# Kernel optimization log

Hardware: AMD Instinct MI355X
Metric: run time of the kernel (lower is better)

Reference implementation:

```python
import jax, jax.numpy as jnp
import numpy as np

N = 50000   # nodes
E = 400000  # edges
H = 4       # heads
C = 64      # hidden per head
IN = 8
G = 64      # graphs in batch
NEG_SLOPE = 0.2


def setup_inputs() -> dict:
    key = jax.random.key(0)
    ks = jax.random.split(key, 32)
    def w(k, shape, fan_in):
        return jax.random.normal(k, shape, jnp.float32) * (1.0 / np.sqrt(fan_in))
    inp = {}
    inp['x'] = jax.random.normal(ks[0], (N, IN), jnp.float32)
    inp['edge_index'] = jax.random.randint(ks[1], (2, E), 0, N, jnp.int32)
    inp['edge_attr'] = jax.random.normal(ks[2], (E, 1), jnp.float32)
    inp['batch'] = jnp.sort(jax.random.randint(ks[3], (N,), 0, G, jnp.int32))
    # encoder
    inp['enc_w'] = w(ks[4], (IN, H * 16), IN)[:, :64]  # [8,64]
    inp['enc_b'] = jnp.zeros((64,), jnp.float32)
    # gat1: in 64 -> H*C = 256
    inp['g1_wl'] = w(ks[5], (64, H * C), 64)
    inp['g1_bl'] = jnp.zeros((H * C,), jnp.float32)
    inp['g1_wr'] = w(ks[6], (64, H * C), 64)
    inp['g1_we'] = w(ks[7], (1, H * C), 1)
    inp['g1_att'] = w(ks[8], (H, C), C)
    inp['g1_b'] = jnp.zeros((H * C,), jnp.float32)
    # gat2: in 256 -> H*C = 256
    inp['g2_wl'] = w(ks[9], (H * C, H * C), H * C)
    inp['g2_bl'] = jnp.zeros((H * C,), jnp.float32)
    inp['g2_wr'] = w(ks[10], (H * C, H * C), H * C)
    inp['g2_we'] = w(ks[11], (1, H * C), 1)
    inp['g2_att'] = w(ks[12], (H, C), C)
    inp['g2_b'] = jnp.zeros((H * C,), jnp.float32)
    # post MLP: 256 -> 128 -> LN -> ReLU -> 128 -> 64 -> ReLU
    inp['p1_w'] = w(ks[13], (H * C, 128), H * C)
    inp['p1_b'] = jnp.zeros((128,), jnp.float32)
    inp['ln_g'] = jnp.ones((128,), jnp.float32)
    inp['ln_b'] = jnp.zeros((128,), jnp.float32)
    inp['p2_w'] = w(ks[14], (128, 64), 128)
    inp['p2_b'] = jnp.zeros((64,), jnp.float32)
    inp['head_w'] = w(ks[15], (64, 1), 64)
    inp['head_b'] = jnp.zeros((1,), jnp.float32)
    return inp


def gatv2_conv(h, src, dst, ea, wl, bl, wr, we, att, b):
    # PyG GATv2Conv (concat=True): message from src j aggregated at dst i
    xl = (h @ wl + bl).reshape(N, H, C)   # lin_l(x_j), carries source messages
    xr = (h @ wr).reshape(N, H, C)        # lin_r(x_i)
    e = (ea @ we).reshape(E, H, C)        # lin_edge(edge_attr)
    s = jax.nn.leaky_relu(xl[src] + xr[dst] + e, NEG_SLOPE)  # [E,H,C]
    logits = jnp.einsum('ehc,hc->eh', s, att)                # [E,H]
    # softmax over incoming edges of each dst node
    mx = jax.ops.segment_max(logits, dst, num_segments=N)
    ex = jnp.exp(logits - mx[dst])
    denom = jax.ops.segment_sum(ex, dst, num_segments=N)
    alpha = ex / (denom[dst] + 1e-16)                        # [E,H]
    out = jax.ops.segment_sum(alpha[:, :, None] * xl[src], dst, num_segments=N)
    return out.reshape(N, H * C) + b


def reference(x, edge_index, edge_attr, batch, enc_w, enc_b,
              g1_wl, g1_bl, g1_wr, g1_we, g1_att, g1_b,
              g2_wl, g2_bl, g2_wr, g2_we, g2_att, g2_b,
              p1_w, p1_b, ln_g, ln_b, p2_w, p2_b, head_w, head_b):
    src, dst = edge_index[0], edge_index[1]
    h = jax.nn.relu(x @ enc_w + enc_b)
    h = jax.nn.relu(gatv2_conv(h, src, dst, edge_attr, g1_wl, g1_bl, g1_wr, g1_we, g1_att, g1_b))
    h = jax.nn.relu(gatv2_conv(h, src, dst, edge_attr, g2_wl, g2_bl, g2_wr, g2_we, g2_att, g2_b))
    # global mean pool per graph
    s = jax.ops.segment_sum(h, batch, num_segments=G)
    cnt = jax.ops.segment_sum(jnp.ones((N,), h.dtype), batch, num_segments=G)
    g = s / jnp.maximum(cnt, 1.0)[:, None]                   # [G, H*C]
    # post MLP (dropout is identity in eval)
    z = g @ p1_w + p1_b
    mu = jnp.mean(z, axis=-1, keepdims=True)
    var = jnp.mean((z - mu) ** 2, axis=-1, keepdims=True)
    z = (z - mu) * jax.lax.rsqrt(var + 1e-5) * ln_g + ln_b
    z = jax.nn.relu(z)
    z = jax.nn.relu(z @ p2_w + p2_b)
    return (z @ head_w + head_b).squeeze(-1)                 # [G]
```

## Files before the change

kernel.cpp:

```cpp
#include <hip/hip_runtime.h>
#include <hip/hip_bf16.h>
#include <math.h>

#define NN 50000
#define NE 400000
#define HH 4
#define CC 64
#define HC 256
#define GG 64
#define NB 196
#define ENCB 12500
#define WCB 640

typedef short v8s __attribute__((ext_vector_type(8)));
typedef float f32x4 __attribute__((ext_vector_type(4)));

static __device__ inline unsigned short f2bf(float v) {
  __hip_bfloat16 b = __float2bfloat16(v);
  return *reinterpret_cast<unsigned short*>(&b);
}
static __device__ inline float bflo(unsigned u) { return __uint_as_float(u << 16); }
static __device__ inline float bfhi(unsigned u) { return __uint_as_float(u & 0xffff0000u); }

__global__ __launch_bounds__(256) void head_kernel(
    const float* __restrict__ x, const float* __restrict__ enc_w,
    const float* __restrict__ enc_b, unsigned short* __restrict__ h0,
    const float* __restrict__ g1_wl, const float* __restrict__ g1_wr,
    const float* __restrict__ g2_wl, const float* __restrict__ g2_wr,
    unsigned short* __restrict__ wt1, unsigned short* __restrict__ wt2,
    const int* __restrict__ batch, int* __restrict__ deg,
    float* __restrict__ pool, int* __restrict__ bounds) {
  int bid = blockIdx.x, tid = threadIdx.x;
  if (bid < ENCB) {
    int idx = bid * 256 + tid;
    int node = idx >> 6, col = idx & 63;
    const float* xr = x + node * 8;
    float acc = enc_b[col];
#pragma unroll
    for (int k = 0; k < 8; ++k) acc += xr[k] * enc_w[k * 64 + col];
    h0[idx] = f2bf(fmaxf(acc, 0.f));
  } else if (bid < ENCB + WCB) {
    int idx = (bid - ENCB) * 256 + tid;
    const float* W; unsigned short* Wt; int K; int base;
    if (idx < 16384)        { W = g1_wl; Wt = wt1;                     K = 64;  base = idx; }
    else if (idx < 32768)   { W = g1_wr; Wt = wt1 + (size_t)256 * 64;  K = 64;  base = idx - 16384; }
    else if (idx < 98304)   { W = g2_wl; Wt = wt2;                     K = 256; base = idx - 32768; }
    else if (idx < 163840)  { W = g2_wr; Wt = wt2 + (size_t)256 * 256; K = 256; base = idx - 98304; }
    else return;
    int k = base >> 8, n = base & 255;
    Wt[n * K + k] = f2bf(W[base]);
  } else {
    int sb = bid - ENCB - WCB;
    int i = sb * 256 + tid;
    if (i < NN) deg[i] = 0;
    if (sb < GG) pool[sb * 256 + tid] = 0.f;
    if (sb == NB - 1 && tid <= GG) {
      int g = tid, lo = 0, hi = NN;
      while (lo < hi) {
        int mid = (lo + hi) >> 1;
        if (batch[mid] < g) lo = mid + 1; else hi = mid;
      }
      bounds[g] = lo;
    }
  }
}

template <int K>
__global__ __launch_bounds__(256) void matmul_mfma_kernel(
    const unsigned short* __restrict__ A, const unsigned short* __restrict__ Wt,
    const float* __restrict__ bias,
    unsigned short* __restrict__ outL, unsigned short* __restrict__ outR, int M) {
  constexpr int AP = 40;
  __shared__ unsigned short a_lds[128 * AP];
  __shared__ unsigned short b_lds[128 * AP];
  const int tid = threadIdx.x;
  const int wave = tid >> 6;
  const int lane = tid & 63;
  const int quad = lane >> 4;
  const int lrow = lane & 15;
  const int wr = (wave & 1) * 64;
  const int wc = (wave >> 1) * 64;
  const int r0 = blockIdx.x * 128;
  const int n0 = blockIdx.y * 128;

  f32x4 acc[4][4];
#pragma unroll
  for (int i = 0; i < 4; ++i)
#pragma unroll
    for (int j = 0; j < 4; ++j) acc[i][j] = (f32x4){0.f, 0.f, 0.f, 0.f};

  const int srow = tid >> 1;
  const int shalf = tid & 1;
  int agrow = r0 + srow; if (agrow >= M) agrow = M - 1;
  const int bgrow = n0 + srow;

  for (int k0 = 0; k0 < K; k0 += 32) {
    {
      const float4* sa = (const float4*)&A[(size_t)agrow * K + k0 + shalf * 16];
      const float4* sb = (const float4*)&Wt[(size_t)bgrow * K + k0 + shalf * 16];
      float4 va0 = sa[0], va1 = sa[1];
      float4 vb0 = sb[0], vb1 = sb[1];
      *(float4*)&a_lds[srow * AP + shalf * 16]     = va0;
      *(float4*)&a_lds[srow * AP + shalf * 16 + 8] = va1;
      *(float4*)&b_lds[srow * AP + shalf * 16]     = vb0;
      *(float4*)&b_lds[srow * AP + shalf * 16 + 8] = vb1;
    }
    __syncthreads();

    v8s af[4], bf[4];
#pragma unroll
    for (int rt = 0; rt < 4; ++rt)
      af[rt] = *(const v8s*)&a_lds[(wr + rt * 16 + lrow) * AP + quad * 8];
#pragma unroll
    for (int ct = 0; ct < 4; ++ct)
      bf[ct] = *(const v8s*)&b_lds[(wc + ct * 16 + lrow) * AP + quad * 8];
#pragma unroll
    for (int rt = 0; rt < 4; ++rt)
#pragma unroll
      for (int ct = 0; ct < 4; ++ct)
        acc[rt][ct] = __builtin_amdgcn_mfma_f32_16x16x32_bf16(af[rt], bf[ct], acc[rt][ct], 0, 0, 0);
    __syncthreads();
  }

  const bool isL = (n0 < 256);
  unsigned short* outp = isL ? outL : outR;
  const int cbase = isL ? n0 : (n0 - 256);
  constexpr int SP = 136;
  unsigned short* stage = a_lds;

#pragma unroll
  for (int rt = 0; rt < 4; ++rt) {
    __syncthreads();
#pragma unroll
    for (int ct = 0; ct < 4; ++ct) {
      int col = wc + ct * 16 + lrow;
      float b = isL ? bias[cbase + col] : 0.f;
#pragma unroll
      for (int r = 0; r < 4; ++r) {
        int sr = (wave & 1) * 16 + quad * 4 + r;
        stage[sr * SP + col] = f2bf(acc[rt][ct][r] + b);
      }
    }
    __syncthreads();
    int sr = tid >> 3;
    int c0 = (tid & 7) * 16;
    int grow = r0 + (sr >> 4) * 64 + rt * 16 + (sr & 15);
    if (grow < M) {
      uint4 v0 = *(const uint4*)&stage[sr * SP + c0];
      uint4 v1 = *(const uint4*)&stage[sr * SP + c0 + 8];
      *(uint4*)&outp[(size_t)grow * 256 + cbase + c0] = v0;
      *(uint4*)&outp[(size_t)grow * 256 + cbase + c0 + 8] = v1;
    }
  }
}

__global__ void degree_kernel(const int* __restrict__ ei, int* __restrict__ deg) {
  int e = blockIdx.x * 256 + threadIdx.x;
  if (e < NE) atomicAdd(&deg[ei[NE + e]], 1);
}

__global__ __launch_bounds__(256) void blocksum_kernel(
    const int* __restrict__ deg, int* __restrict__ bsum) {
  int t = threadIdx.x;
  int i = blockIdx.x * 256 + t;
  int v = (i < NN) ? deg[i] : 0;
#pragma unroll
  for (int off = 32; off; off >>= 1) v += __shfl_down(v, off, 64);
  __shared__ int ws[4];
  if ((t & 63) == 0) ws[t >> 6] = v;
  __syncthreads();
  if (t == 0) bsum[blockIdx.x] = ws[0] + ws[1] + ws[2] + ws[3];
}

__global__ __launch_bounds__(256) void blockscan_kernel(
    const int* __restrict__ bsum, int* __restrict__ bpre, int* __restrict__ rowstart) {
  __shared__ int s[256];
  int t = threadIdx.x;
  int v = (t < NB) ? bsum[t] : 0;
  s[t] = v;
  __syncthreads();
  for (int off = 1; off < 256; off <<= 1) {
    int x = s[t];
    int y = (t >= off) ? s[t - off] : 0;
    __syncthreads();
    s[t] = x + y;
    __syncthreads();
  }
  if (t < NB) bpre[t] = s[t] - v;
  if (t == 255) rowstart[NN] = s[255];
}

__global__ __launch_bounds__(256) void rowstart_kernel(
    const int* __restrict__ deg, const int* __restrict__ bpre,
    int* __restrict__ rowstart, int* __restrict__ cursor) {
  __shared__ int s[256];
  int t = threadIdx.x;
  int i = blockIdx.x * 256 + t;
  int v = (i < NN) ? deg[i] : 0;
  s[t] = v;
  __syncthreads();
  for (int off = 1; off < 256; off <<= 1) {
    int x = s[t];
    int y = (t >= off) ? s[t - off] : 0;
    __syncthreads();
    s[t] = x + y;
    __syncthreads();
  }
  if (i < NN) {
    int rs = bpre[blockIdx.x] + s[t] - v;
    rowstart[i] = rs;
    cursor[i] = rs;
  }
}

__global__ void fill_kernel(const int* __restrict__ ei, const float* __restrict__ ea,
                            int* __restrict__ cursor, int2* __restrict__ edges) {
  int e = blockIdx.x * 256 + threadIdx.x;
  if (e < NE) {
    int d = ei[NE + e];
    int pos = atomicAdd(&cursor[d], 1);
    edges[pos] = make_int2(ei[e] << 9, __float_as_int(ea[e]));
  }
}

__global__ __launch_bounds__(256) void gat_fused_kernel(
    const int* __restrict__ rowstart, const int2* __restrict__ edges,
    const unsigned short* __restrict__ xl, const unsigned short* __restrict__ xr,
    const float* __restrict__ we, const float* __restrict__ att,
    const float* __restrict__ bias, unsigned short* __restrict__ outb) {
  int node = (blockIdx.x * 256 + threadIdx.x) >> 6;
  int lane = threadIdx.x & 63;
  int r0 = __builtin_amdgcn_readfirstlane(rowstart[node]);
  int r1 = __builtin_amdgcn_readfirstlane(rowstart[node + 1]);
  const char* xlp = (const char*)xl + lane * 8;
  uint2 rp = ((const uint2*)xr)[(size_t)node * 64 + lane];
  float4 r = make_float4(bflo(rp.x), bfhi(rp.x), bflo(rp.y), bfhi(rp.y));
  float4 wv = ((const float4*)we)[lane];
  float4 at = ((const float4*)att)[lane];
  const float LOG2E = 1.442695040888963f;
  at.x *= LOG2E; at.y *= LOG2E; at.z *= LOG2E; at.w *= LOG2E;
  float4 acc = make_float4(0.f, 0.f, 0.f, 0.f);
  float denom = 0.f;

  auto edge_step = [&](float eav, uint2 p) {
    float4 a = make_float4(bflo(p.x), bfhi(p.x), bflo(p.y), bfhi(p.y));
    float s0 = a.x + (r.x + eav * wv.x);
    float s1 = a.y + (r.y + eav * wv.y);
    float s2 = a.z + (r.z + eav * wv.z);
    float s3 = a.w + (r.w + eav * wv.w);
    s0 = fmaxf(s0, 0.2f * s0);
    s1 = fmaxf(s1, 0.2f * s1);
    s2 = fmaxf(s2, 0.2f * s2);
    s3 = fmaxf(s3, 0.2f * s3);
    float p4 = (s0 * at.x + s1 * at.y) + (s2 * at.z + s3 * at.w);
#pragma unroll
    for (int off = 8; off; off >>= 1) p4 += __shfl_xor(p4, off, 16);
    float ex = exp2f(p4);
    denom += ex;
    acc.x += ex * a.x; acc.y += ex * a.y; acc.z += ex * a.z; acc.w += ex * a.w;
  };

  int i = r0;
  for (; i + 4 <= r1; i += 4) {
    int2 e0 = edges[i];     int2 e1 = edges[i + 1];
    int2 e2 = edges[i + 2]; int2 e3 = edges[i + 3];
    uint2 p0 = *(const uint2*)(xlp + (unsigned)e0.x);
    uint2 p1 = *(const uint2*)(xlp + (unsigned)e1.x);
    uint2 p2 = *(const uint2*)(xlp + (unsigned)e2.x);
    uint2 p3 = *(const uint2*)(xlp + (unsigned)e3.x);
    edge_step(__int_as_float(e0.y), p0);
    edge_step(__int_as_float(e1.y), p1);
    edge_step(__int_as_float(e2.y), p2);
    edge_step(__int_as_float(e3.y), p3);
  }
  for (; i < r1; ++i) {
    int2 e = edges[i];
    edge_step(__int_as_float(e.y), *(const uint2*)(xlp + (unsigned)e.x));
  }

  float inv = 1.f / (denom + 1e-16f);
  float4 bv = ((const float4*)bias)[lane];
  float4 o;
  o.x = fmaxf(acc.x * inv + bv.x, 0.f);
  o.y = fmaxf(acc.y * inv + bv.y, 0.f);
  o.z = fmaxf(acc.z * inv + bv.z, 0.f);
  o.w = fmaxf(acc.w * inv + bv.w, 0.f);
  uint2 pk;
  pk.x = (unsigned)f2bf(o.x) | ((unsigned)f2bf(o.y) << 16);
  pk.y = (unsigned)f2bf(o.z) | ((unsigned)f2bf(o.w) << 16);
  ((uint2*)outb)[(size_t)node * 64 + lane] = pk;
}

__global__ __launch_bounds__(256) void pool_kernel(
    const unsigned short* __restrict__ h, const int* __restrict__ batch,
    float* __restrict__ pool) {
  int rg = threadIdx.x >> 6;
  int lane = threadIdx.x & 63;
  int n0 = blockIdx.x * 64;
  const uint2* h2 = (const uint2*)h;
  float4 acc = make_float4(0.f, 0.f, 0.f, 0.f);
  int cur = -1;
#pragma unroll 4
  for (int i = 0; i < 16; ++i) {
    int n = n0 + rg + 4 * i;
    if (n >= NN) break;
    int b = batch[n];
    if (b != cur) {
      if (cur >= 0) {
        float* p = &pool[cur * 256 + lane * 4];
        atomicAdd(p + 0, acc.x); atomicAdd(p + 1, acc.y);
        atomicAdd(p + 2, acc.z); atomicAdd(p + 3, acc.w);
      }
      cur = b;
      acc = make_float4(0.f, 0.f, 0.f, 0.f);
    }
    uint2 v = h2[(size_t)n * 64 + lane];
    acc.x += bflo(v.x); acc.y += bfhi(v.x);
    acc.z += bflo(v.y); acc.w += bfhi(v.y);
  }
  if (cur >= 0) {
    float* p = &pool[cur * 256 + lane * 4];
    atomicAdd(p + 0, acc.x); atomicAdd(p + 1, acc.y);
    atomicAdd(p + 2, acc.z); atomicAdd(p + 3, acc.w);
  }
}

__global__ __launch_bounds__(128) void mlp_kernel(
    const float* __restrict__ pool, const int* __restrict__ bounds,
    const float* __restrict__ p1w, const float* __restrict__ p1b,
    const float* __restrict__ lng, const float* __restrict__ lnb,
    const float* __restrict__ p2w, const float* __restrict__ p2b,
    const float* __restrict__ hw, const float* __restrict__ hb,
    float* __restrict__ out) {
  __shared__ float sg[256];
  __shared__ float red[128];
  __shared__ float sz[128];
  __shared__ float s2[64];
  int b = blockIdx.x, tid = threadIdx.x;
  float cntf = (float)(bounds[b + 1] - bounds[b]);
  float invc = 1.f / fmaxf(cntf, 1.f);
  for (int i = tid; i < 256; i += 128) sg[i] = pool[b * 256 + i] * invc;
  __syncthreads();
  float z = p1b[tid];
  for (int k = 0; k < 256; ++k) z += sg[k] * p1w[k * 128 + tid];
  red[tid] = z; __syncthreads();
  for (int off = 64; off; off >>= 1) { if (tid < off) red[tid] += red[tid + off]; __syncthreads(); }
  float mu = red[0] * (1.f / 128.f);
  __syncthreads();
  float d = z - mu;
  red[tid] = d * d; __syncthreads();
  for (int off = 64; off; off >>= 1) { if (tid < off) red[tid] += red[tid + off]; __syncthreads(); }
  float var = red[0] * (1.f / 128.f);
  float zn = d * rsqrtf(var + 1e-5f) * lng[tid] + lnb[tid];
  sz[tid] = fmaxf(zn, 0.f);
  __syncthreads();
  if (tid < 64) {
    float a = p2b[tid];
    for (int k = 0; k < 128; ++k) a += sz[k] * p2w[k * 64 + tid];
    s2[tid] = fmaxf(a, 0.f);
  }
  __syncthreads();
  if (tid < 64) {
    float p = s2[tid] * hw[tid];
    for (int off = 32; off; off >>= 1) p += __shfl_down(p, off, 64);
    if (tid == 0) out[b] = p + hb[0];
  }
}

extern "C" void kernel_launch(void* const* d_in, const int* in_sizes, int n_in,
                              void* d_out, int out_size, void* d_ws, size_t ws_size,
                              hipStream_t stream) {
  const float* x      = (const float*)d_in[0];
  const int*   ei     = (const int*)d_in[1];
  const float* ea     = (const float*)d_in[2];
  const int*   batch  = (const int*)d_in[3];
  const float* enc_w  = (const float*)d_in[4];
  const float* enc_b  = (const float*)d_in[5];
  const float* g1_wl  = (const float*)d_in[6];
  const float* g1_bl  = (const float*)d_in[7];
  const float* g1_wr  = (const float*)d_in[8];
  const float* g1_we  = (const float*)d_in[9];
  const float* g1_att = (const float*)d_in[10];
  const float* g1_b   = (const float*)d_in[11];
  const float* g2_wl  = (const float*)d_in[12];
  const float* g2_bl  = (const float*)d_in[13];
  const float* g2_wr  = (const float*)d_in[14];
  const float* g2_we  = (const float*)d_in[15];
  const float* g2_att = (const float*)d_in[16];
  const float* g2_b   = (const float*)d_in[17];
  const float* p1_w   = (const float*)d_in[18];
  const float* p1_b   = (const float*)d_in[19];
  const float* ln_g   = (const float*)d_in[20];
  const float* ln_b   = (const float*)d_in[21];
  const float* p2_w   = (const float*)d_in[22];
  const float* p2_b   = (const float*)d_in[23];
  const float* head_w = (const float*)d_in[24];
  const float* head_b = (const float*)d_in[25];
  float* out = (float*)d_out;

  char* ws = (char*)d_ws;
  size_t off = 0;
  auto alloc = [&](size_t bytes) -> void* {
    void* p = ws + off;
    off = (off + bytes + 255) & ~(size_t)255;
    return p;
  };
  unsigned short* xl   = (unsigned short*)alloc((size_t)NN * HC * 2);
  unsigned short* xr   = (unsigned short*)alloc((size_t)NN * HC * 2);
  unsigned short* h0   = (unsigned short*)alloc((size_t)NN * 64 * 2);
  unsigned short* hb16 = (unsigned short*)alloc((size_t)NN * HC * 2);
  unsigned short* wt1  = (unsigned short*)alloc((size_t)512 * 64 * 2);
  unsigned short* wt2  = (unsigned short*)alloc((size_t)512 * 256 * 2);
  float* pool      = (float*)alloc((size_t)GG * HC * 4);
  int*   deg       = (int*)alloc((size_t)NN * 4);
  int*   rowstart  = (int*)alloc((size_t)(NN + 1) * 4);
  int*   cursor    = (int*)alloc((size_t)NN * 4);
  int*   bsum      = (int*)alloc((size_t)NB * 4);
  int*   bpre      = (int*)alloc((size_t)NB * 4);
  int2*  edges     = (int2*)alloc((size_t)NE * 8);
  int*   bounds    = (int*)alloc((size_t)(GG + 1) * 4);

  head_kernel<<<ENCB + WCB + NB, 256, 0, stream>>>(
      x, enc_w, enc_b, h0, g1_wl, g1_wr, g2_wl, g2_wr, wt1, wt2,
      batch, deg, pool, bounds);

  degree_kernel<<<(NE + 255) / 256, 256, 0, stream>>>(ei, deg);
  blocksum_kernel<<<NB, 256, 0, stream>>>(deg, bsum);
  blockscan_kernel<<<1, 256, 0, stream>>>(bsum, bpre, rowstart);
  rowstart_kernel<<<NB, 256, 0, stream>>>(deg, bpre, rowstart, cursor);
  fill_kernel<<<(NE + 255) / 256, 256, 0, stream>>>(ei, ea, cursor, edges);

  dim3 mmg((NN + 127) / 128, 4);

  matmul_mfma_kernel<64><<<mmg, 256, 0, stream>>>(h0, wt1, g1_bl, xl, xr, NN);
  gat_fused_kernel<<<NN / 4, 256, 0, stream>>>(rowstart, edges, xl, xr,
                                               g1_we, g1_att, g1_b, hb16);

  matmul_mfma_kernel<256><<<mmg, 256, 0, stream>>>(hb16, wt2, g2_bl, xl, xr, NN);
  gat_fused_kernel<<<NN / 4, 256, 0, stream>>>(rowstart, edges, xl, xr,
                                               g2_we, g2_att, g2_b, hb16);

  pool_kernel<<<(NN + 63) / 64, 256, 0, stream>>>(hb16, batch, pool);
  mlp_kernel<<<GG, 128, 0, stream>>>(pool, bounds, p1_w, p1_b, ln_g, ln_b,
                                     p2_w, p2_b, head_w, head_b, out);
}
```

Before: 338.4 us.

## Use direct global-to-LDS loads with swizzle, XCD block remap, fuse edge fill into matmul

The matmul now stages A and W tiles through global_load_lds straight into a swizzled, unpadded LDS layout instead of round-tripping through registers. Block IDs are remapped so that consecutive tiles land on the same XCD, which should improve L2 reuse. The CSR edge-fill kernel is folded into the first matmul launch as extra blocks, removing one launch and letting the two run concurrently. The cost is more complex indexing and reliance on the swizzle and LDS-load semantics being correct.

After: 337.1 us. No clear change (-0.4%).

```diff
diff --git a/kernel.cpp b/kernel.cpp
--- a/kernel.cpp
+++ b/kernel.cpp
@@ -21,6 +21,12 @@
 }
 static __device__ inline float bflo(unsigned u) { return __uint_as_float(u << 16); }
 static __device__ inline float bfhi(unsigned u) { return __uint_as_float(u & 0xffff0000u); }
+
+static __device__ inline void gload_lds16(const void* g, void* l) {
+  __builtin_amdgcn_global_load_lds(
+      (const __attribute__((address_space(1))) void*)g,
+      (__attribute__((address_space(3))) void*)l, 16, 0, 0);
+}
 
 __global__ __launch_bounds__(256) void head_kernel(
     const float* __restrict__ x, const float* __restrict__ enc_w,
@@ -65,14 +71,30 @@
   }
 }
 
-template <int K>
+template <int K, bool FILL>
 __global__ __launch_bounds__(256) void matmul_mfma_kernel(
     const unsigned short* __restrict__ A, const unsigned short* __restrict__ Wt,
     const float* __restrict__ bias,
-    unsigned short* __restrict__ outL, unsigned short* __restrict__ outR, int M) {
-  constexpr int AP = 40;
-  __shared__ unsigned short a_lds[128 * AP];
-  __shared__ unsigned short b_lds[128 * AP];
+    unsigned short* __restrict__ outL, unsigned short* __restrict__ outR, int M,
+    const int* __restrict__ ei, const float* __restrict__ ea,
+    int* __restrict__ cursor, int2* __restrict__ edges) {
+  const int mmb = ((M + 127) >> 7) << 2;
+  int bid = blockIdx.x;
+  if (FILL && bid >= mmb) {
+    int e = (bid - mmb) * 256 + threadIdx.x;
+    if (e < NE) {
+      int d = ei[NE + e];
+      int pos = atomicAdd(&cursor[d], 1);
+      edges[pos] = make_int2(ei[e] << 9, __float_as_int(ea[e]));
+    }
+    return;
+  }
+  {
+    int q = mmb >> 3, r = mmb & 7;
+    int xcd = bid & 7, off2 = bid >> 3;
+    bid = (xcd < r ? xcd * (q + 1) : r * (q + 1) + (xcd - r) * q) + off2;
+  }
+  __shared__ __attribute__((aligned(16))) unsigned short lds[8192];
   const int tid = threadIdx.x;
   const int wave = tid >> 6;
   const int lane = tid & 63;
@@ -80,8 +102,8 @@
   const int lrow = lane & 15;
   const int wr = (wave & 1) * 64;
   const int wc = (wave >> 1) * 64;
-  const int r0 = blockIdx.x * 128;
-  const int n0 = blockIdx.y * 128;
+  const int r0 = (bid >> 2) * 128;
+  const int n0 = (bid & 3) * 128;
 
   f32x4 acc[4][4];
 #pragma unroll
@@ -89,31 +111,37 @@
 #pragma unroll
     for (int j = 0; j < 4; ++j) acc[i][j] = (f32x4){0.f, 0.f, 0.f, 0.f};
 
-  const int srow = tid >> 1;
-  const int shalf = tid & 1;
-  int agrow = r0 + srow; if (agrow >= M) agrow = M - 1;
-  const int bgrow = n0 + srow;
+  const int lrA0 = (wave * 2) * 16 + (lane >> 2);
+  const int lrA1 = lrA0 + 16;
+  const int c    = lane & 3;
+  const int cs0  = c ^ ((lrA0 >> 1) & 3);
+  const int cs1  = c ^ ((lrA1 >> 1) & 3);
+  int ga0 = r0 + lrA0; if (ga0 >= M) ga0 = M - 1;
+  int ga1 = r0 + lrA1; if (ga1 >= M) ga1 = M - 1;
+  const unsigned short* srcA0 = A  + (size_t)ga0 * K + cs0 * 8;
+  const unsigned short* srcA1 = A  + (size_t)ga1 * K + cs1 * 8;
+  const unsigned short* srcB0 = Wt + (size_t)(n0 + lrA0) * K + cs0 * 8;
+  const unsigned short* srcB1 = Wt + (size_t)(n0 + lrA1) * K + cs1 * 8;
+  unsigned short* dA0 = &lds[(wave * 2 + 0) * 512];
+  unsigned short* dA1 = &lds[(wave * 2 + 1) * 512];
+  unsigned short* dB0 = &lds[4096 + (wave * 2 + 0) * 512];
+  unsigned short* dB1 = &lds[4096 + (wave * 2 + 1) * 512];
+  const int qsw = (quad ^ ((lrow >> 1) & 3)) * 8;
 
   for (int k0 = 0; k0 < K; k0 += 32) {
-    {
-      const float4* sa = (const float4*)&A[(size_t)agrow * K + k0 + shalf * 16];
-      const float4* sb = (const float4*)&Wt[(size_t)bgrow * K + k0 + shalf * 16];
-      float4 va0 = sa[0], va1 = sa[1];
-      float4 vb0 = sb[0], vb1 = sb[1];
-      *(float4*)&a_lds[srow * AP + shalf * 16]     = va0;
-      *(float4*)&a_lds[srow * AP + shalf * 16 + 8] = va1;
-      *(float4*)&b_lds[srow * AP + shalf * 16]     = vb0;
-      *(float4*)&b_lds[srow * AP + shalf * 16 + 8] = vb1;
-    }
+    gload_lds16(srcA0 + k0, dA0);
+    gload_lds16(srcA1 + k0, dA1);
+    gload_lds16(srcB0 + k0, dB0);
+    gload_lds16(srcB1 + k0, dB1);
     __syncthreads();
 
     v8s af[4], bf[4];
 #pragma unroll
     for (int rt = 0; rt < 4; ++rt)
-      af[rt] = *(const v8s*)&a_lds[(wr + rt * 16 + lrow) * AP + quad * 8];
+      af[rt] = *(const v8s*)&lds[(wr + rt * 16 + lrow) * 32 + qsw];
 #pragma unroll
     for (int ct = 0; ct < 4; ++ct)
-      bf[ct] = *(const v8s*)&b_lds[(wc + ct * 16 + lrow) * AP + quad * 8];
+      bf[ct] = *(const v8s*)&lds[4096 + (wc + ct * 16 + lrow) * 32 + qsw];
 #pragma unroll
     for (int rt = 0; rt < 4; ++rt)
 #pragma unroll
@@ -126,7 +154,7 @@
   unsigned short* outp = isL ? outL : outR;
   const int cbase = isL ? n0 : (n0 - 256);
   constexpr int SP = 136;
-  unsigned short* stage = a_lds;
+  unsigned short* stage = lds;
 
 #pragma unroll
   for (int rt = 0; rt < 4; ++rt) {
@@ -210,16 +238,6 @@
     int rs = bpre[blockIdx.x] + s[t] - v;
     rowstart[i] = rs;
     cursor[i] = rs;
-  }
-}
-
-__global__ void fill_kernel(const int* __restrict__ ei, const float* __restrict__ ea,
-                            int* __restrict__ cursor, int2* __restrict__ edges) {
-  int e = blockIdx.x * 256 + threadIdx.x;
-  if (e < NE) {
-    int d = ei[NE + e];
-    int pos = atomicAdd(&cursor[d], 1);
-    edges[pos] = make_int2(ei[e] << 9, __float_as_int(ea[e]));
   }
 }
 
@@ -428,15 +446,17 @@
   blocksum_kernel<<<NB, 256, 0, stream>>>(deg, bsum);
   blockscan_kernel<<<1, 256, 0, stream>>>(bsum, bpre, rowstart);
   rowstart_kernel<<<NB, 256, 0, stream>>>(deg, bpre, rowstart, cursor);
-  fill_kernel<<<(NE + 255) / 256, 256, 0, stream>>>(ei, ea, cursor, edges);
-
-  dim3 mmg((NN + 127) / 128, 4);
-
-  matmul_mfma_kernel<64><<<mmg, 256, 0, stream>>>(h0, wt1, g1_bl, xl, xr, NN);
+
+  const int MMB = ((NN + 127) / 128) * 4;
+  const int FB  = (NE + 255) / 256;
+
+  matmul_mfma_kernel<64, true><<<MMB + FB, 256, 0, stream>>>(
+      h0, wt1, g1_bl, xl, xr, NN, ei, ea, cursor, edges);
   gat_fused_kernel<<<NN / 4, 256, 0, stream>>>(rowstart, edges, xl, xr,
                                                g1_we, g1_att, g1_b, hb16);
 
-  matmul_mfma_kernel<256><<<mmg, 256, 0, stream>>>(hb16, wt2, g2_bl, xl, xr, NN);
+  matmul_mfma_kernel<256, false><<<MMB, 256, 0, stream>>>(
+      hb16, wt2, g2_bl, xl, xr, NN, nullptr, nullptr, nullptr, nullptr);
   gat_fused_kernel<<<NN / 4, 256, 0, stream>>>(rowstart, edges, xl, xr,
                                                g2_we, g2_att, g2_b, hb16);
 
```
